# Optimization experiments

Measured on AMD Instinct MI355X. Metric: run time of the kernel, lower is better.

The kernel has to match this reference:

```python
import jax, jax.numpy as jnp
import numpy as np

DIM, DH, H_HEADS, F, HH, WW = 512, 64, 8, 16, 32, 32
FF_IN = int(DIM * 4 * 2 / 3)  # 1365


def _ln(x, w, b):
    m = x.mean(-1, keepdims=True)
    v = ((x - m) ** 2).mean(-1, keepdims=True)
    return (x - m) * jax.lax.rsqrt(v + 1e-5) * w + b


def _attn(x, ln_w, ln_b, wq, wkv, nkv, nbias, wout, oln_w, oln_b, rel_bias):
    # x: (B, N, D); K/V are single-head (shared across heads) per the source to_kv
    B, N, D = x.shape
    H = nbias.shape[0]
    dh = nkv.shape[-1]
    xn = _ln(x, ln_w, ln_b)
    q = (xn @ wq).reshape(B, N, H, dh).transpose(0, 2, 1, 3) * (dh ** -0.5)
    k, v = jnp.split(xn @ wkv, 2, axis=-1)  # (B, N, dh) each
    nk = jnp.broadcast_to(nkv[0], (B, 1, dh))
    nv = jnp.broadcast_to(nkv[1], (B, 1, dh))
    k = jnp.concatenate([nk, k], axis=1)  # (B, N+1, dh)
    v = jnp.concatenate([nv, v], axis=1)
    sim = jnp.einsum('bhid,bjd->bhij', q, k)  # (B, H, N, N+1)
    bias = jnp.concatenate([jnp.broadcast_to(nbias[:, None, None], (H, N, 1)), rel_bias], axis=-1)
    attn = jax.nn.softmax(sim + bias[None], axis=-1)
    out = jnp.einsum('bhij,bjd->bhid', attn, v)
    out = out.transpose(0, 2, 1, 3).reshape(B, N, H * dh)
    return _ln(out @ wout, oln_w, oln_b)


def _cpb_mlp(coords, w0, b0, w1, b1, w2, b2):
    t = jax.nn.silu(coords @ w0 + b0)
    t = jax.nn.silu(t @ w1 + b1)
    return t @ w2 + b2  # (R, heads)


def _spatial_bias(h, w, w0, b0, w1, b1, w2, b2):
    rh = jnp.arange(-h + 1, h)
    rw = jnp.arange(-w + 1, w)
    gh, gw = jnp.meshgrid(rh, rw, indexing='ij')
    coords = jnp.stack([gh, gw], axis=-1).reshape(-1, 2).astype(jnp.float32)
    table = _cpb_mlp(coords, w0, b0, w1, b1, w2, b2)  # ((2h-1)(2w-1), H)
    ph, pw = jnp.meshgrid(jnp.arange(h), jnp.arange(w), indexing='ij')
    p = jnp.stack([ph, pw], axis=-1).reshape(-1, 2)  # (hw, 2)
    rel = p[:, None] - p[None]  # (hw, hw, 2)
    idx = (rel[..., 0] + h - 1) * (2 * w - 1) + (rel[..., 1] + w - 1)
    return table[idx].transpose(2, 0, 1)  # (H, hw, hw)


def _temporal_bias(f, w0, b0, w1, b1, w2, b2):
    coords = jnp.arange(-f + 1, f, dtype=jnp.float32)[:, None]
    table = _cpb_mlp(coords, w0, b0, w1, b1, w2, b2)  # (2f-1, H)
    idx = jnp.arange(f)[:, None] - jnp.arange(f)[None] + f - 1
    return table[idx].transpose(2, 0, 1)  # (H, f, f)


def _ff(x, win, g, wout):
    # 1x1x1 conv == channel matmul; GEGLU; shift_token; ChanLayerNorm; conv out
    y = jnp.einsum('bcfhw,cd->bdfhw', x, win)
    a, gate = jnp.split(y, 2, axis=1)
    y = a * jax.nn.gelu(gate, approximate=False)
    c = y.shape[1]
    c1 = (c + 1) // 2  # torch.chunk: first chunk gets ceil
    y1, y2 = y[:, :c1], y[:, c1:]
    y2 = jnp.pad(y2, ((0, 0), (0, 0), (1, 0), (0, 0), (0, 0)))[:, :, :-1]
    y = jnp.concatenate([y1, y2], axis=1)
    m = y.mean(1, keepdims=True)
    v = ((y - m) ** 2).mean(1, keepdims=True)
    y = (y - m) * jax.lax.rsqrt(jnp.maximum(v, 1e-5)) * g.reshape(1, -1, 1, 1, 1)
    return jnp.einsum('bcfhw,cd->bdfhw', y, wout)


def setup_inputs() -> dict:
    key = jax.random.key(0)
    ks = jax.random.split(key, 32)
    d2 = DIM // 2
    inner = DH * H_HEADS

    def nrm(k, shape, s=0.02):
        return jax.random.normal(k, shape, jnp.float32) * s

    inp = {'x': jax.random.normal(ks[0], (1, DIM, F, HH, WW), jnp.float32)}
    for pre, i in (('sa', 1), ('ta', 11)):
        inp[pre + '_ln_w'] = jnp.ones(DIM, jnp.float32)
        inp[pre + '_ln_b'] = jnp.zeros(DIM, jnp.float32)
        inp[pre + '_wq'] = nrm(ks[i], (DIM, inner))
        inp[pre + '_wkv'] = nrm(ks[i + 1], (DIM, 2 * DH))
        inp[pre + '_null_kv'] = nrm(ks[i + 2], (2, DH), 1.0)
        inp[pre + '_null_bias'] = nrm(ks[i + 3], (H_HEADS,), 1.0)
        inp[pre + '_wout'] = nrm(ks[i + 4], (inner, DIM))
        inp[pre + '_oln_w'] = jnp.ones(DIM, jnp.float32)
        inp[pre + '_oln_b'] = jnp.zeros(DIM, jnp.float32)
    inp['sp_w0'] = nrm(ks[20], (2, d2), 0.1); inp['sp_b0'] = jnp.zeros(d2, jnp.float32)
    inp['sp_w1'] = nrm(ks[21], (d2, d2), 0.05); inp['sp_b1'] = jnp.zeros(d2, jnp.float32)
    inp['sp_w2'] = nrm(ks[22], (d2, H_HEADS), 0.05); inp['sp_b2'] = jnp.zeros(H_HEADS, jnp.float32)
    inp['tp_w0'] = nrm(ks[23], (1, d2), 0.1); inp['tp_b0'] = jnp.zeros(d2, jnp.float32)
    inp['tp_w1'] = nrm(ks[24], (d2, d2), 0.05); inp['tp_b1'] = jnp.zeros(d2, jnp.float32)
    inp['tp_w2'] = nrm(ks[25], (d2, H_HEADS), 0.05); inp['tp_b2'] = jnp.zeros(H_HEADS, jnp.float32)
    inp['ff_win'] = nrm(ks[26], (DIM, 2 * FF_IN))
    inp['ff_g'] = jnp.ones(FF_IN, jnp.float32)
    inp['ff_wout'] = nrm(ks[27], (FF_IN, DIM))
    return inp


def _forward(x, sa_ln_w, sa_ln_b, sa_wq, sa_wkv, sa_null_kv, sa_null_bias, sa_wout, sa_oln_w, sa_oln_b,
             ta_ln_w, ta_ln_b, ta_wq, ta_wkv, ta_null_kv, ta_null_bias, ta_wout, ta_oln_w, ta_oln_b,
             sp_w0, sp_b0, sp_w1, sp_b1, sp_w2, sp_b2,
             tp_w0, tp_b0, tp_w1, tp_b1, tp_w2, tp_b2,
             ff_win, ff_g, ff_wout):
    b, c, f, h, w = x.shape
    # spatial attention over (h*w) tokens, batched over (b*f)
    xs = x.transpose(0, 2, 3, 4, 1).reshape(b * f, h * w, c)
    sb = _spatial_bias(h, w, sp_w0, sp_b0, sp_w1, sp_b1, sp_w2, sp_b2)
    xs = _attn(xs, sa_ln_w, sa_ln_b, sa_wq, sa_wkv, sa_null_kv, sa_null_bias, sa_wout, sa_oln_w, sa_oln_b, sb) + xs
    xv = xs.reshape(b, f, h, w, c).transpose(0, 4, 1, 2, 3)
    # temporal attention over f tokens, batched over (b*h*w)
    xt = xv.transpose(0, 3, 4, 2, 1).reshape(b * h * w, f, c)
    tb = _temporal_bias(f, tp_w0, tp_b0, tp_w1, tp_b1, tp_w2, tp_b2)
    xt = _attn(xt, ta_ln_w, ta_ln_b, ta_wq, ta_wkv, ta_null_kv, ta_null_bias, ta_wout, ta_oln_w, ta_oln_b, tb) + xt
    xv = xt.reshape(b, h, w, f, c).transpose(0, 4, 3, 1, 2)
    # feed-forward with token shift
    return _ff(xv, ff_win, ff_g, ff_wout) + xv


def reference(x, sa_ln_w, sa_ln_b, sa_wq, sa_wkv, sa_null_kv, sa_null_bias, sa_wout, sa_oln_w, sa_oln_b,
              ta_ln_w, ta_ln_b, ta_wq, ta_wkv, ta_null_kv, ta_null_bias, ta_wout, ta_oln_w, ta_oln_b,
              sp_w0, sp_b0, sp_w1, sp_b1, sp_w2, sp_b2,
              tp_w0, tp_b0, tp_w1, tp_b1, tp_w2, tp_b2,
              ff_win, ff_g, ff_wout):
    return _forward(x, sa_ln_w, sa_ln_b, sa_wq, sa_wkv, sa_null_kv, sa_null_bias, sa_wout, sa_oln_w, sa_oln_b,
                    ta_ln_w, ta_ln_b, ta_wq, ta_wkv, ta_null_kv, ta_null_bias, ta_wout, ta_oln_w, ta_oln_b,
                    sp_w0, sp_b0, sp_w1, sp_b1, sp_w2, sp_b2,
                    tp_w0, tp_b0, tp_w1, tp_b1, tp_w2, tp_b2,
                    ff_win, ff_g, ff_wout)
```

## Files before the change

### kernel.cpp

```cpp
#include <hip/hip_runtime.h>
#include <math.h>

#define TOK 16384
#define DIMC 512
#define FFI 1365
#define CH1 683
#define YSLD 1376
#define KVPAD 1056
#define BSTRIDE 1152
#define MASKB (-30000.f)

typedef unsigned int u32;
typedef unsigned short ushort_t;
typedef __attribute__((ext_vector_type(8))) short bf16x8;
typedef __attribute__((ext_vector_type(4))) float f32x4;

__device__ inline ushort_t f2b(float x) {
    u32 u = __float_as_uint(x);
    u32 r = (u + 0x7fffu + ((u >> 16) & 1u)) >> 16;
    return (ushort_t)r;
}
__device__ inline float b2f(ushort_t u) { return __uint_as_float(((u32)u) << 16); }

__device__ inline void gload_lds16(const void* g, void* l) {
    __builtin_amdgcn_global_load_lds(
        (const __attribute__((address_space(1))) u32*)g,
        (__attribute__((address_space(3))) u32*)l, 16, 0, 0);
}

__device__ inline float gelu_exact(float x) {
    return 0.5f * x * (1.f + erff(x * 0.70710678118654752f));
}

__global__ __launch_bounds__(256) void cpb_kernel(
    const float* __restrict__ w0, const float* __restrict__ b0,
    const float* __restrict__ w1, const float* __restrict__ b1,
    const float* __restrict__ w2, const float* __restrict__ b2,
    float* __restrict__ table, int mode)
{
    __shared__ float t0[256];
    __shared__ float t1[256];
    int r = blockIdx.x;
    int t = threadIdx.x;
    float c0, c1;
    if (mode == 0) { c0 = (float)(r / 63 - 31); c1 = (float)(r % 63 - 31); }
    else           { c0 = (float)(r - 15);      c1 = 0.f; }
    float a = c0 * w0[t] + b0[t];
    if (mode == 0) a += c1 * w0[256 + t];
    t0[t] = a / (1.f + __expf(-a));
    __syncthreads();
    float s = b1[t];
    for (int k = 0; k < 256; ++k) s += t0[k] * w1[k * 256 + t];
    t1[t] = s / (1.f + __expf(-s));
    __syncthreads();
    if (t < 8) {
        float o = b2[t];
        for (int k = 0; k < 256; ++k) o += t1[k] * w2[k * 8 + t];
        table[r * 8 + t] = o;
    }
}

__global__ __launch_bounds__(256) void bias_sp_kernel(
    const float* __restrict__ tab, const float* __restrict__ nullbias,
    ushort_t* __restrict__ out)
{
    int pi = blockIdx.x, h = blockIdx.y;
    int phi = pi >> 5, pwi = pi & 31;
    ushort_t* row = out + ((size_t)h * 1024 + pi) * BSTRIDE;
    for (int c = threadIdx.x; c < BSTRIDE; c += 256) {
        float v;
        if (c == 0) v = nullbias[h];
        else if (c <= 1024) {
            int pj = c - 1;
            int phj = pj >> 5, pwj = pj & 31;
            int idx = (phi - phj + 31) * 63 + (pwi - pwj + 31);
            v = tab[idx * 8 + h];
        } else v = MASKB;
        row[c] = f2b(v);
    }
}

__global__ __launch_bounds__(256) void kvinit_kernel(
    const float* __restrict__ nullkv, ushort_t* __restrict__ KP, ushort_t* __restrict__ VT)
{
    int f = blockIdx.x, t = threadIdx.x;
    for (int e = t; e < 32 * 64; e += 256) {
        int rr = e >> 6, d = e & 63;
        int row = (rr == 0) ? 0 : (1024 + rr);
        KP[((size_t)f * KVPAD + row) * 64 + d] = (rr == 0) ? f2b(nullkv[d]) : (ushort_t)0;
    }
    for (int e = t; e < 64 * 32; e += 256) {
        int d = e >> 5, cc = e & 31;
        int col = (cc == 0) ? 0 : (1024 + cc);
        VT[((size_t)f * 64 + d) * KVPAD + col] = (cc == 0) ? f2b(nullkv[64 + d]) : (ushort_t)0;
    }
}

__global__ __launch_bounds__(256) void wcvt_kernel(
    const float* __restrict__ W, int ldw, int c0,
    ushort_t* __restrict__ Bt, int Kp, int K, int Ncols,
    const float* __restrict__ gv, int Nwrite)
{
    __shared__ float tile[32][33];
    int nb = blockIdx.x * 32, kb = blockIdx.y * 32;
    int tx = threadIdx.x & 31, ty = threadIdx.x >> 5;
    #pragma unroll
    for (int it = 0; it < 4; ++it) {
        int k = kb + ty + it * 8, n = nb + tx;
        float v = (k < K && n < Ncols) ? W[(size_t)k * ldw + c0 + n] : 0.f;
        if (gv && k < K) v *= gv[k];
        tile[ty + it * 8][tx] = v;
    }
    __syncthreads();
    #pragma unroll
    for (int it = 0; it < 4; ++it) {
        int n = nb + ty + it * 8, k = kb + tx;
        if (n < Nwrite && k < Kp) Bt[(size_t)n * Kp + k] = f2b(tile[tx][ty + it * 8]);
    }
}

__global__ __launch_bounds__(256) void transpose_in_kernel(
    const float* __restrict__ x, float* __restrict__ dst)
{
    __shared__ float tile[32][33];
    int t0b = blockIdx.x * 32, c0b = blockIdx.y * 32;
    int tx = threadIdx.x & 31, ty = threadIdx.x >> 5;
    #pragma unroll
    for (int it = 0; it < 4; ++it) {
        int c = ty + it * 8;
        tile[c][tx] = x[(size_t)(c0b + c) * TOK + t0b + tx];
    }
    __syncthreads();
    #pragma unroll
    for (int it = 0; it < 4; ++it) {
        int tr = ty + it * 8;
        dst[(size_t)(t0b + tr) * DIMC + c0b + tx] = tile[tx][tr];
    }
}

__global__ __launch_bounds__(256) void ln_bf16_kernel(
    const float* __restrict__ in, ushort_t* __restrict__ out,
    const float* __restrict__ w, const float* __restrict__ b)
{
    __shared__ float r1[4], r2[4];
    size_t base = (size_t)blockIdx.x * DIMC;
    int t = threadIdx.x;
    float x0 = in[base + t], x1 = in[base + 256 + t];
    float s = x0 + x1, s2 = x0 * x0 + x1 * x1;
    #pragma unroll
    for (int o = 32; o > 0; o >>= 1) { s += __shfl_down(s, o, 64); s2 += __shfl_down(s2, o, 64); }
    if ((t & 63) == 0) { r1[t >> 6] = s; r2[t >> 6] = s2; }
    __syncthreads();
    float mean = (r1[0] + r1[1] + r1[2] + r1[3]) * (1.f / 512.f);
    float ex2  = (r2[0] + r2[1] + r2[2] + r2[3]) * (1.f / 512.f);
    float rstd = rsqrtf(ex2 - mean * mean + 1e-5f);
    out[base + t]       = f2b((x0 - mean) * rstd * w[t] + b[t]);
    out[base + 256 + t] = f2b((x1 - mean) * rstd * w[256 + t] + b[256 + t]);
}

__global__ __launch_bounds__(256) void ln_add_kernel(
    const float* __restrict__ proj, float* __restrict__ io,
    const float* __restrict__ w, const float* __restrict__ b)
{
    __shared__ float r1[4], r2[4];
    size_t base = (size_t)blockIdx.x * DIMC;
    int t = threadIdx.x;
    float x0 = proj[base + t], x1 = proj[base + 256 + t];
    float s = x0 + x1, s2 = x0 * x0 + x1 * x1;
    #pragma unroll
    for (int o = 32; o > 0; o >>= 1) { s += __shfl_down(s, o, 64); s2 += __shfl_down(s2, o, 64); }
    if ((t & 63) == 0) { r1[t >> 6] = s; r2[t >> 6] = s2; }
    __syncthreads();
    float mean = (r1[0] + r1[1] + r1[2] + r1[3]) * (1.f / 512.f);
    float ex2  = (r2[0] + r2[1] + r2[2] + r2[3]) * (1.f / 512.f);
    float rstd = rsqrtf(ex2 - mean * mean + 1e-5f);
    io[base + t]       += (x0 - mean) * rstd * w[t] + b[t];
    io[base + 256 + t] += (x1 - mean) * rstd * w[256 + t] + b[256 + t];
}

__global__ __launch_bounds__(128) void permute0_kernel(
    const float* __restrict__ src, float* __restrict__ dst)
{
    int rd = blockIdx.x;
    int rs = (rd & 15) * 1024 + (rd >> 4);
    ((float4*)(dst + (size_t)rd * DIMC))[threadIdx.x] =
        ((const float4*)(src + (size_t)rs * DIMC))[threadIdx.x];
}

__global__ __launch_bounds__(128) void permute1_dual_kernel(
    const float* __restrict__ src, float* __restrict__ dst, ushort_t* __restrict__ dstb)
{
    int rd = blockIdx.x;
    int rs = (rd & 1023) * 16 + (rd >> 10);
    float4 v = ((const float4*)(src + (size_t)rs * DIMC))[threadIdx.x];
    ((float4*)(dst + (size_t)rd * DIMC))[threadIdx.x] = v;
    u32 lo = (u32)f2b(v.x) | ((u32)f2b(v.y) << 16);
    u32 hi = (u32)f2b(v.z) | ((u32)f2b(v.w) << 16);
    ((uint2*)(dstb + (size_t)rd * DIMC))[threadIdx.x] = make_uint2(lo, hi);
}

template<int EPI>
__global__ __launch_bounds__(256) void gemm_mfma(
    const ushort_t* __restrict__ A, int lda,
    const ushort_t* __restrict__ Bt, int Kp,
    float* __restrict__ C, ushort_t* __restrict__ Cb, int ldc,
    int M, int N, int K, float scale, int nx,
    const float* __restrict__ stats, const float* __restrict__ g,
    const float* __restrict__ resid, float* __restrict__ outT,
    ushort_t* __restrict__ KPo, ushort_t* __restrict__ VTo)
{
    __shared__ __align__(16) ushort_t As[4 * 128 * 8];
    __shared__ __align__(16) ushort_t Bs[4 * 128 * 8];
    int lin = blockIdx.x;
    int xcd = lin & 7, idx = lin >> 3;
    int m0 = (xcd * 16 + (idx & 15)) * 128;
    int n0 = (idx >> 4) * 128;
    int tid = threadIdx.x, lane = tid & 63, wid = tid >> 6;
    int wy = wid >> 1, wx = wid & 1, quad = lane >> 4, l16 = lane & 15;
    bool bfull = (n0 + 128 <= N);
    f32x4 acc[4][4];
    #pragma unroll
    for (int i = 0; i < 4; ++i)
        #pragma unroll
        for (int j = 0; j < 4; ++j) { acc[i][j][0]=0.f; acc[i][j][1]=0.f; acc[i][j][2]=0.f; acc[i][j][3]=0.f; }

    for (int k0 = 0; k0 < K; k0 += 32) {
        if (k0) __syncthreads();
        #pragma unroll
        for (int r = 0; r < 2; ++r) {
            int c = wid * 128 + r * 64 + lane;
            const ushort_t* src = A + (size_t)(m0 + (c & 127)) * lda + k0 + (c >> 7) * 8;
            gload_lds16(src, &As[(wid * 128 + r * 64) * 8]);
        }
        if (bfull) {
            #pragma unroll
            for (int r = 0; r < 2; ++r) {
                int c = wid * 128 + r * 64 + lane;
                const ushort_t* src = Bt + (size_t)(n0 + (c & 127)) * Kp + k0 + (c >> 7) * 8;
                gload_lds16(src, &Bs[(wid * 128 + r * 64) * 8]);
            }
        } else {
            #pragma unroll
            for (int r = 0; r < 2; ++r) {
                int c = tid + r * 256;
                int kg = c >> 7, nloc = c & 127;
                bf16x8 v;
                if (n0 + nloc < N) v = *(const bf16x8*)(Bt + (size_t)(n0 + nloc) * Kp + k0 + kg * 8);
                else { for (int e = 0; e < 8; ++e) v[e] = 0; }
                *(bf16x8*)&Bs[c * 8] = v;
            }
        }
        __syncthreads();
        bf16x8 af[4], bfr[4];
        #pragma unroll
        for (int i = 0; i < 4; ++i) af[i] = *(bf16x8*)&As[(quad * 128 + wy * 64 + i * 16 + l16) * 8];
        #pragma unroll
        for (int j = 0; j < 4; ++j) bfr[j] = *(bf16x8*)&Bs[(quad * 128 + wx * 64 + j * 16 + l16) * 8];
        #pragma unroll
        for (int i = 0; i < 4; ++i)
            #pragma unroll
            for (int j = 0; j < 4; ++j)
                acc[i][j] = __builtin_amdgcn_mfma_f32_16x16x32_bf16(af[i], bfr[j], acc[i][j], 0, 0, 0);
    }
    #pragma unroll
    for (int i = 0; i < 4; ++i) {
        #pragma unroll
        for (int j = 0; j < 4; ++j) {
            #pragma unroll
            for (int r = 0; r < 4; ++r) {
                int m = m0 + wy * 64 + i * 16 + quad * 4 + r;
                int n = n0 + wx * 64 + j * 16 + l16;
                if (n >= N) continue;
                float v = acc[i][j][r] * scale;
                if (EPI == 0) {
                    C[(size_t)m * ldc + n] = v;
                } else if (EPI == 3) {
                    Cb[(size_t)m * ldc + n] = f2b(v);
                } else if (EPI == 4) {
                    int frame = m >> 10, tt = m & 1023;
                    if (n < 64) KPo[((size_t)frame * KVPAD + 1 + tt) * 64 + n] = f2b(v);
                    else        VTo[((size_t)frame * 64 + (n - 64)) * KVPAD + 1 + tt] = f2b(v);
                } else if (EPI == 5) {
                    float s0 = stats[2 * m], s1 = stats[2 * m + 1];
                    outT[(size_t)n * TOK + m] = v * s1 - s0 * g[n] + resid[(size_t)m * DIMC + n];
                }
            }
        }
    }
}

__global__ __launch_bounds__(256) void ff_gemm_fused(
    const ushort_t* __restrict__ A,
    const ushort_t* __restrict__ BI,
    ushort_t* __restrict__ YS)
{
    __shared__ __align__(16) ushort_t As[4 * 128 * 8];
    __shared__ __align__(16) ushort_t Bs[4 * 2 * 64 * 8];
    int lin = blockIdx.x;
    int xcd = lin & 7, idx = lin >> 3;
    int m0 = (xcd * 16 + (idx & 15)) * 128;
    int n0 = (idx >> 4) * 64;
    int tid = threadIdx.x, lane = tid & 63, wid = tid >> 6;
    int wy = wid >> 1, wx = wid & 1, quad = lane >> 4, l16 = lane & 15;
    f32x4 aA[4][2], aG[4][2];
    #pragma unroll
    for (int i = 0; i < 4; ++i)
        #pragma unroll
        for (int j = 0; j < 2; ++j) {
            aA[i][j][0]=0.f; aA[i][j][1]=0.f; aA[i][j][2]=0.f; aA[i][j][3]=0.f;
            aG[i][j][0]=0.f; aG[i][j][1]=0.f; aG[i][j][2]=0.f; aG[i][j][3]=0.f;
        }

    for (int k0 = 0; k0 < 512; k0 += 32) {
        if (k0) __syncthreads();
        #pragma unroll
        for (int r = 0; r < 2; ++r) {
            int c = wid * 128 + r * 64 + lane;
            gload_lds16(A + (size_t)(m0 + (c & 127)) * 512 + k0 + (c >> 7) * 8,
                        &As[(wid * 128 + r * 64) * 8]);
        }
        #pragma unroll
        for (int r = 0; r < 2; ++r) {
            gload_lds16(BI + (size_t)((n0 + lane) * 2 + r) * 512 + k0 + wid * 8,
                        &Bs[(wid * 128 + r * 64) * 8]);
        }
        __syncthreads();
        bf16x8 af[4], ba[2], bg[2];
        #pragma unroll
        for (int i = 0; i < 4; ++i) af[i] = *(bf16x8*)&As[(quad * 128 + wy * 64 + i * 16 + l16) * 8];
        #pragma unroll
        for (int j = 0; j < 2; ++j) {
            int nn = wx * 32 + j * 16 + l16;
            ba[j] = *(bf16x8*)&Bs[(quad * 128 + nn) * 8];
            bg[j] = *(bf16x8*)&Bs[(quad * 128 + 64 + nn) * 8];
        }
        #pragma unroll
        for (int i = 0; i < 4; ++i)
            #pragma unroll
            for (int j = 0; j < 2; ++j) {
                aA[i][j] = __builtin_amdgcn_mfma_f32_16x16x32_bf16(af[i], ba[j], aA[i][j], 0, 0, 0);
                aG[i][j] = __builtin_amdgcn_mfma_f32_16x16x32_bf16(af[i], bg[j], aG[i][j], 0, 0, 0);
            }
    }
    #pragma unroll
    for (int i = 0; i < 4; ++i) {
        #pragma unroll
        for (int j = 0; j < 2; ++j) {
            #pragma unroll
            for (int r = 0; r < 4; ++r) {
                int m = m0 + wy * 64 + i * 16 + quad * 4 + r;
                int n = n0 + wx * 32 + j * 16 + l16;
                if (n >= FFI) {
                    if (n < YSLD) YS[(size_t)m * YSLD + n] = 0;
                    continue;
                }
                float v = aA[i][j][r] * gelu_exact(aG[i][j][r]);
                int dr = (n < CH1) ? m : m + 1024;
                if (dr < TOK) YS[(size_t)dr * YSLD + n] = f2b(v);
                if (n >= CH1 && m < 1024) YS[(size_t)m * YSLD + n] = 0;
            }
        }
    }
}

__global__ __launch_bounds__(256) void attn_sp_mfma(
    const ushort_t* __restrict__ Q,
    const ushort_t* __restrict__ KP,
    const ushort_t* __restrict__ VT,
    const ushort_t* __restrict__ BIASX,
    ushort_t* __restrict__ O)
{
    __shared__ __align__(16) ushort_t Ks[128 * 64];
    __shared__ __align__(16) ushort_t Vs[64 * 128];
    __shared__ __align__(16) ushort_t PT[4][16 * 136];
    int lin = blockIdx.x;
    int xcd = lin & 7, idx = lin >> 3;
    int qt = xcd * 8 + (idx & 7);
    int frame = idx >> 3;
    int q0 = qt * 16;
    int tid = threadIdx.x, lane = tid & 63, wid = tid >> 6;
    int quad = lane >> 4, l16 = lane & 15;
    ushort_t* PTw = &PT[wid][0];

    bf16x8 aQ[2][2];
    const ushort_t* brow[2];
    #pragma unroll
    for (int i = 0; i < 2; ++i) {
        int h = wid * 2 + i;
        const ushort_t* qp = Q + (size_t)(frame * 1024 + q0 + l16) * 512 + h * 64 + quad * 8;
        aQ[i][0] = *(const bf16x8*)qp;
        aQ[i][1] = *(const bf16x8*)(qp + 32);
        brow[i] = BIASX + ((size_t)h * 1024 + q0 + l16) * BSTRIDE;
    }
    f32x4 Oc[2][4];
    float mcol[2], lcol[2];
    #pragma unroll
    for (int i = 0; i < 2; ++i) {
        #pragma unroll
        for (int nt = 0; nt < 4; ++nt) { Oc[i][nt][0]=0.f; Oc[i][nt][1]=0.f; Oc[i][nt][2]=0.f; Oc[i][nt][3]=0.f; }
        mcol[i] = -1.0e30f; lcol[i] = 0.f;
    }

    for (int jt = 0; jt < 9; ++jt) {
        __syncthreads();
        #pragma unroll
        for (int r = 0; r < 4; ++r) {
            int L = wid * 256 + r * 64 + lane;
            int c = L >> 3, gp = L & 7, gg = gp ^ (c & 7);
            int jj = jt * 128 + c; if (jj > KVPAD - 1) jj = KVPAD - 1;
            gload_lds16(KP + ((size_t)frame * KVPAD + jj) * 64 + gg * 8, &Ks[(wid * 256 + r * 64) * 8]);
        }
        #pragma unroll
        for (int r = 0; r < 4; ++r) {
            int L = wid * 256 + r * 64 + lane;
            int d = L >> 4, cgp = L & 15;
            int cg = (cgp & 8) | ((cgp & 7) ^ (d & 7));
            int col = jt * 128 + cg * 8; if (col > KVPAD - 8) col = KVPAD - 8;
            gload_lds16(VT + ((size_t)frame * 64 + d) * KVPAD + col, &Vs[(wid * 256 + r * 64) * 8]);
        }
        __syncthreads();
        f32x4 S[2][8];
        #pragma unroll
        for (int i = 0; i < 2; ++i)
            #pragma unroll
            for (int j = 0; j < 8; ++j) { S[i][j][0]=0.f; S[i][j][1]=0.f; S[i][j][2]=0.f; S[i][j][3]=0.f; }
        #pragma unroll
        for (int j = 0; j < 8; ++j) {
            int c = j * 16 + l16;
            #pragma unroll
            for (int ks = 0; ks < 2; ++ks) {
                bf16x8 kb = *(bf16x8*)&Ks[(c * 8 + ((ks * 4 + quad) ^ (c & 7))) * 8];
                S[0][j] = __builtin_amdgcn_mfma_f32_16x16x32_bf16(kb, aQ[0][ks], S[0][j], 0, 0, 0);
                S[1][j] = __builtin_amdgcn_mfma_f32_16x16x32_bf16(kb, aQ[1][ks], S[1][j], 0, 0, 0);
            }
        }
        #pragma unroll
        for (int i = 0; i < 2; ++i) {
            #pragma unroll
            for (int j = 0; j < 8; ++j) {
                int kbase = jt * 128 + j * 16 + quad * 4;
                uint2 bv = *(const uint2*)(brow[i] + kbase);
                S[i][j][0] += b2f((ushort_t)(bv.x & 0xffffu));
                S[i][j][1] += b2f((ushort_t)(bv.x >> 16));
                S[i][j][2] += b2f((ushort_t)(bv.y & 0xffffu));
                S[i][j][3] += b2f((ushort_t)(bv.y >> 16));
            }
        }
        float alpha[2];
        #pragma unroll
        for (int i = 0; i < 2; ++i) {
            float mx = S[i][0][0];
            #pragma unroll
            for (int j = 0; j < 8; ++j)
                #pragma unroll
                for (int r = 0; r < 4; ++r) mx = fmaxf(mx, S[i][j][r]);
            mx = fmaxf(mx, __shfl_xor(mx, 16, 64));
            mx = fmaxf(mx, __shfl_xor(mx, 32, 64));
            float mnew = fmaxf(mcol[i], mx);
            alpha[i] = __expf(mcol[i] - mnew);
            mcol[i] = mnew;
            float rs = 0.f;
            #pragma unroll
            for (int j = 0; j < 8; ++j)
                #pragma unroll
                for (int r = 0; r < 4; ++r) {
                    float p = __expf(S[i][j][r] - mnew);
                    S[i][j][r] = p;
                    rs += p;
                }
            rs += __shfl_xor(rs, 16, 64);
            rs += __shfl_xor(rs, 32, 64);
            lcol[i] = lcol[i] * alpha[i] + rs;
        }
        #pragma unroll
        for (int i = 0; i < 2; ++i) {
            #pragma unroll
            for (int r = 0; r < 4; ++r) {
                float ar = __shfl(alpha[i], quad * 4 + r, 64);
                #pragma unroll
                for (int nt = 0; nt < 4; ++nt) Oc[i][nt][r] *= ar;
            }
        }
        #pragma unroll
        for (int i = 0; i < 2; ++i) {
            #pragma unroll
            for (int j = 0; j < 8; ++j) {
                u32 u0 = __float_as_uint(S[i][j][0]) + 0x8000u;
                u32 u1 = __float_as_uint(S[i][j][1]) + 0x8000u;
                u32 u2 = __float_as_uint(S[i][j][2]) + 0x8000u;
                u32 u3 = __float_as_uint(S[i][j][3]) + 0x8000u;
                uint2 pk;
                pk.x = (u0 >> 16) | (u1 & 0xffff0000u);
                pk.y = (u2 >> 16) | (u3 & 0xffff0000u);
                *(uint2*)&PTw[l16 * 136 + j * 16 + quad * 4] = pk;
            }
            #pragma unroll
            for (int ks = 0; ks < 4; ++ks) {
                bf16x8 pa = *(bf16x8*)&PTw[l16 * 136 + ks * 32 + quad * 8];
                #pragma unroll
                for (int nt = 0; nt < 4; ++nt) {
                    int d = nt * 16 + l16;
                    int cg = ks * 4 + quad;
                    int phys = (cg & 8) | ((cg & 7) ^ (d & 7));
                    bf16x8 vb = *(bf16x8*)&Vs[(d * 16 + phys) * 8];
                    Oc[i][nt] = __builtin_amdgcn_mfma_f32_16x16x32_bf16(pa, vb, Oc[i][nt], 0, 0, 0);
                }
            }
        }
    }
    #pragma unroll
    for (int i = 0; i < 2; ++i) {
        int h = wid * 2 + i;
        #pragma unroll
        for (int r = 0; r < 4; ++r) {
            float linv = 1.f / __shfl(lcol[i], quad * 4 + r, 64);
            int ql = quad * 4 + r;
            #pragma unroll
            for (int nt = 0; nt < 4; ++nt) {
                int d = nt * 16 + l16;
                O[(size_t)(frame * 1024 + q0 + ql) * 512 + h * 64 + d] = f2b(Oc[i][nt][r] * linv);
            }
        }
    }
}

__global__ __launch_bounds__(256) void attn_tp_kernel(
    const ushort_t* __restrict__ q, const ushort_t* __restrict__ kv,
    const float* __restrict__ nullkv, const float* __restrict__ nullbias,
    const float* __restrict__ table, ushort_t* __restrict__ out)
{
    __shared__ float qs[16][512];
    __shared__ float ks[17][64];
    __shared__ float vs[17][64];
    __shared__ float sc[8][16][17];
    int b = blockIdx.x;
    int t = threadIdx.x;
    for (int e = t; e < 16 * 512; e += 256) {
        int f = e >> 9, c = e & 511;
        qs[f][c] = b2f(q[(size_t)(b * 16 + f) * 512 + c]);
    }
    for (int e = t; e < 17 * 64; e += 256) {
        int j = e >> 6, d = e & 63;
        ks[j][d] = (j == 0) ? nullkv[d]      : b2f(kv[(size_t)(b * 16 + j - 1) * 128 + d]);
        vs[j][d] = (j == 0) ? nullkv[64 + d] : b2f(kv[(size_t)(b * 16 + j - 1) * 128 + 64 + d]);
    }
    __syncthreads();
    for (int e = t; e < 8 * 16 * 17; e += 256) {
        int h = e / 272, rem = e - h * 272;
        int i = rem / 17, j = rem - i * 17;
        float acc = 0.f;
        for (int d = 0; d < 64; ++d) acc += qs[i][h * 64 + d] * ks[j][d];
        float bias = (j == 0) ? nullbias[h] : table[(i - (j - 1) + 15) * 8 + h];
        sc[h][i][j] = acc + bias;
    }
    __syncthreads();
    if (t < 128) {
        int h = t >> 4, i = t & 15;
        float mx = -1e30f;
        for (int j = 0; j < 17; ++j) mx = fmaxf(mx, sc[h][i][j]);
        float s = 0.f;
        for (int j = 0; j < 17; ++j) { float p = __expf(sc[h][i][j] - mx); sc[h][i][j] = p; s += p; }
        float inv = 1.f / s;
        for (int j = 0; j < 17; ++j) sc[h][i][j] *= inv;
    }
    __syncthreads();
    for (int e = t; e < 16 * 512; e += 256) {
        int i = e >> 9, c = e & 511;
        int h = c >> 6, d = c & 63;
        float acc = 0.f;
        #pragma unroll
        for (int j = 0; j < 17; ++j) acc += sc[h][i][j] * vs[j][d];
        out[(size_t)(b * 16 + i) * 512 + c] = f2b(acc);
    }
}

__global__ __launch_bounds__(256) void rowstats_bf16_kernel(
    const ushort_t* __restrict__ YS, float* __restrict__ stats)
{
    __shared__ float r1[4], r2[4];
    int r = blockIdx.x, t = threadIdx.x;
    const ushort_t* row = YS + (size_t)r * YSLD;
    float s = 0.f, s2 = 0.f;
    for (int c = t; c < FFI; c += 256) {
        float v = b2f(row[c]);
        s += v; s2 += v * v;
    }
    #pragma unroll
    for (int o = 32; o > 0; o >>= 1) { s += __shfl_down(s, o, 64); s2 += __shfl_down(s2, o, 64); }
    if ((t & 63) == 0) { r1[t >> 6] = s; r2[t >> 6] = s2; }
    __syncthreads();
    float S  = r1[0] + r1[1] + r1[2] + r1[3];
    float S2 = r2[0] + r2[1] + r2[2] + r2[3];
    float mean = S * (1.f / 1365.f);
    float var  = S2 * (1.f / 1365.f) - mean * mean;
    float rstd = rsqrtf(fmaxf(var, 1e-5f));
    if (t == 0) { stats[2 * r] = mean * rstd; stats[2 * r + 1] = rstd; }
}

__global__ __launch_bounds__(64) void colsum_kernel(
    const ushort_t* __restrict__ Wt, float* __restrict__ colsum)
{
    int n = blockIdx.x, t = threadIdx.x;
    const ushort_t* row = Wt + (size_t)n * YSLD;
    float s = 0.f;
    for (int k = t; k < YSLD; k += 64) s += b2f(row[k]);
    #pragma unroll
    for (int o = 32; o > 0; o >>= 1) s += __shfl_down(s, o, 64);
    if (t == 0) colsum[n] = s;
}

extern "C" void kernel_launch(void* const* d_in, const int* in_sizes, int n_in,
                              void* d_out, int out_size, void* d_ws, size_t ws_size,
                              hipStream_t stream)
{
    const float* x          = (const float*)d_in[0];
    const float* sa_ln_w    = (const float*)d_in[1];
    const float* sa_ln_b    = (const float*)d_in[2];
    const float* sa_wq      = (const float*)d_in[3];
    const float* sa_wkv     = (const float*)d_in[4];
    const float* sa_null_kv = (const float*)d_in[5];
    const float* sa_null_b  = (const float*)d_in[6];
    const float* sa_wout    = (const float*)d_in[7];
    const float* sa_oln_w   = (const float*)d_in[8];
    const float* sa_oln_b   = (const float*)d_in[9];
    const float* ta_ln_w    = (const float*)d_in[10];
    const float* ta_ln_b    = (const float*)d_in[11];
    const float* ta_wq      = (const float*)d_in[12];
    const float* ta_wkv     = (const float*)d_in[13];
    const float* ta_null_kv = (const float*)d_in[14];
    const float* ta_null_b  = (const float*)d_in[15];
    const float* ta_wout    = (const float*)d_in[16];
    const float* ta_oln_w   = (const float*)d_in[17];
    const float* ta_oln_b   = (const float*)d_in[18];
    const float* sp_w0      = (const float*)d_in[19];
    const float* sp_b0      = (const float*)d_in[20];
    const float* sp_w1      = (const float*)d_in[21];
    const float* sp_b1      = (const float*)d_in[22];
    const float* sp_w2      = (const float*)d_in[23];
    const float* sp_b2      = (const float*)d_in[24];
    const float* tp_w0      = (const float*)d_in[25];
    const float* tp_b0      = (const float*)d_in[26];
    const float* tp_w1      = (const float*)d_in[27];
    const float* tp_b1      = (const float*)d_in[28];
    const float* tp_w2      = (const float*)d_in[29];
    const float* tp_b2      = (const float*)d_in[30];
    const float* ff_win     = (const float*)d_in[31];
    const float* ff_g       = (const float*)d_in[32];
    const float* ff_wout    = (const float*)d_in[33];

    char* ws = (char*)d_ws;
    float*    RES   = (float*)(ws + 0);
    ushort_t* XN16  = (ushort_t*)(ws + 33554432);
    ushort_t* Q16   = (ushort_t*)(ws + 50331648);
    float*    RT    = (float*)(ws + 50331648);
    ushort_t* YS    = (ushort_t*)(ws + 50331648);
    ushort_t* WSA   = (ushort_t*)(ws + 67108864);
    ushort_t* KP    = (ushort_t*)(ws + 83886080);
    ushort_t* VTb   = (ushort_t*)(ws + 86048768);
    ushort_t* KV16  = (ushort_t*)(ws + 83886080);
    ushort_t* WTA   = (ushort_t*)(ws + 90439680);
    ushort_t* AO16  = (ushort_t*)(ws + 92274688);
    ushort_t* BI    = (ushort_t*)(ws + 96468992);
    ushort_t* WFFB  = (ushort_t*)(ws + 99352576);
    ushort_t* BIAS16= (ushort_t*)(ws + 109051904);
    float*    PRJ   = (float*)(ws + 109051904);
    ushort_t* Q16t  = (ushort_t*)(ws + 109051904);
    float*    STATS = (float*)(ws + 142606336);
    float*    SPT   = (float*)(ws + 142737408);
    float*    COLSUM= (float*)(ws + 142737408);
    float*    TPT   = (float*)(ws + 142864448);

    ushort_t* WQ_T  = WSA;
    ushort_t* WKV_T = WSA + 262144;
    ushort_t* WO_T  = WSA + 327680;
    ushort_t* tWQ_T  = WTA;
    ushort_t* tWKV_T = WTA + 262144;
    ushort_t* tWO_T  = WTA + 327680;

    dim3 blk(256);

    cpb_kernel<<<dim3(3969), blk, 0, stream>>>(sp_w0, sp_b0, sp_w1, sp_b1, sp_w2, sp_b2, SPT, 0);
    cpb_kernel<<<dim3(31),   blk, 0, stream>>>(tp_w0, tp_b0, tp_w1, tp_b1, tp_w2, tp_b2, TPT, 1);
    bias_sp_kernel<<<dim3(1024, 8), blk, 0, stream>>>(SPT, sa_null_b, BIAS16);
    kvinit_kernel<<<dim3(16), blk, 0, stream>>>(sa_null_kv, KP, VTb);

    wcvt_kernel<<<dim3(16, 16), blk, 0, stream>>>(sa_wq, 512, 0, WQ_T, 512, 512, 512, nullptr, 512);
    wcvt_kernel<<<dim3(4, 16),  blk, 0, stream>>>(sa_wkv, 128, 0, WKV_T, 512, 512, 128, nullptr, 128);
    wcvt_kernel<<<dim3(16, 16), blk, 0, stream>>>(sa_wout, 512, 0, WO_T, 512, 512, 512, nullptr, 512);
    transpose_in_kernel<<<dim3(512, 16), blk, 0, stream>>>(x, RES);
    ln_bf16_kernel<<<dim3(TOK), blk, 0, stream>>>(RES, XN16, sa_ln_w, sa_ln_b);
    gemm_mfma<3><<<dim3(512), blk, 0, stream>>>(XN16, 512, WQ_T, 512,
        nullptr, Q16, 512, TOK, 512, 512, 0.125f, 4, nullptr, nullptr, nullptr, nullptr, nullptr, nullptr);
    gemm_mfma<4><<<dim3(128), blk, 0, stream>>>(XN16, 512, WKV_T, 512,
        nullptr, nullptr, 0, TOK, 128, 512, 1.0f, 1, nullptr, nullptr, nullptr, nullptr, KP, VTb);
    attn_sp_mfma<<<dim3(1024), blk, 0, stream>>>(Q16, KP, VTb, BIAS16, AO16);
    gemm_mfma<0><<<dim3(512), blk, 0, stream>>>(AO16, 512, WO_T, 512,
        PRJ, nullptr, 512, TOK, 512, 512, 1.0f, 4, nullptr, nullptr, nullptr, nullptr, nullptr, nullptr);
    ln_add_kernel<<<dim3(TOK), blk, 0, stream>>>(PRJ, RES, sa_oln_w, sa_oln_b);

    permute0_kernel<<<dim3(TOK), dim3(128), 0, stream>>>(RES, RT);
    wcvt_kernel<<<dim3(16, 16), blk, 0, stream>>>(ta_wq, 512, 0, tWQ_T, 512, 512, 512, nullptr, 512);
    wcvt_kernel<<<dim3(4, 16),  blk, 0, stream>>>(ta_wkv, 128, 0, tWKV_T, 512, 512, 128, nullptr, 128);
    wcvt_kernel<<<dim3(16, 16), blk, 0, stream>>>(ta_wout, 512, 0, tWO_T, 512, 512, 512, nullptr, 512);
    ln_bf16_kernel<<<dim3(TOK), blk, 0, stream>>>(RT, XN16, ta_ln_w, ta_ln_b);
    gemm_mfma<3><<<dim3(512), blk, 0, stream>>>(XN16, 512, tWQ_T, 512,
        nullptr, Q16t, 512, TOK, 512, 512, 0.125f, 4, nullptr, nullptr, nullptr, nullptr, nullptr, nullptr);
    gemm_mfma<3><<<dim3(128), blk, 0, stream>>>(XN16, 512, tWKV_T, 512,
        nullptr, KV16, 128, TOK, 128, 512, 1.0f, 1, nullptr, nullptr, nullptr, nullptr, nullptr, nullptr);
    attn_tp_kernel<<<dim3(1024), blk, 0, stream>>>(Q16t, KV16, ta_null_kv, ta_null_b, TPT, AO16);
    gemm_mfma<0><<<dim3(512), blk, 0, stream>>>(AO16, 512, tWO_T, 512,
        PRJ, nullptr, 512, TOK, 512, 512, 1.0f, 4, nullptr, nullptr, nullptr, nullptr, nullptr, nullptr);
    ln_add_kernel<<<dim3(TOK), blk, 0, stream>>>(PRJ, RT, ta_oln_w, ta_oln_b);
    permute1_dual_kernel<<<dim3(TOK), dim3(128), 0, stream>>>(RT, RES, XN16);

    wcvt_kernel<<<dim3(44, 16), blk, 0, stream>>>(ff_win, 2730, 0,   BI,       1024, 512, FFI, nullptr, 1408);
    wcvt_kernel<<<dim3(44, 16), blk, 0, stream>>>(ff_win, 2730, FFI, BI + 512, 1024, 512, FFI, nullptr, 1408);
    wcvt_kernel<<<dim3(16, 43), blk, 0, stream>>>(ff_wout, 512, 0, WFFB, YSLD, FFI, 512, ff_g, 512);
    colsum_kernel<<<dim3(512), dim3(64), 0, stream>>>(WFFB, COLSUM);
    ff_gemm_fused<<<dim3(2816), blk, 0, stream>>>(XN16, BI, YS);
    rowstats_bf16_kernel<<<dim3(TOK), blk, 0, stream>>>(YS, STATS);
    gemm_mfma<5><<<dim3(512), blk, 0, stream>>>(YS, YSLD, WFFB, YSLD,
        nullptr, nullptr, 0, TOK, 512, YSLD, 1.0f, 4, STATS, COLSUM, RES, (float*)d_out, nullptr, nullptr);
}
```

Baseline: 919.5 us.

## Use base-2 softmax and register-permuted P in spatial attention kernel

Folds log2(e) into the query scale and the precomputed bias tables so that both attention kernels can use the raw v_exp_f32 instruction instead of __expf. In the spatial attention kernel, the softmax probabilities are no longer staged through shared memory. They are rearranged into the MFMA A-operand layout with ds_bpermute, which removes the PT LDS buffer. The kernel now processes one head at a time to cut live registers, adds s_setprio around the MFMA blocks, and sets a launch-bounds occupancy hint. The costs are extra cross-lane permute instructions, and the log2(e) scaling of the bias is rounded to bf16.

```diff
diff --git a/kernel.cpp b/kernel.cpp
--- a/kernel.cpp
+++ b/kernel.cpp
@@ -9,6 +9,7 @@
 #define KVPAD 1056
 #define BSTRIDE 1152
 #define MASKB (-30000.f)
+#define LOG2E 1.4426950408889634f
 
 typedef unsigned int u32;
 typedef unsigned short ushort_t;
@@ -21,6 +22,12 @@
     return (ushort_t)r;
 }
 __device__ inline float b2f(ushort_t u) { return __uint_as_float(((u32)u) << 16); }
+
+__device__ inline float exp2_fast(float x) {
+    float r;
+    asm("v_exp_f32 %0, %1" : "=v"(r) : "v"(x));
+    return r;
+}
 
 __device__ inline void gload_lds16(const void* g, void* l) {
     __builtin_amdgcn_global_load_lds(
@@ -76,7 +83,7 @@
             int idx = (phi - phj + 31) * 63 + (pwi - pwj + 31);
             v = tab[idx * 8 + h];
         } else v = MASKB;
-        row[c] = f2b(v);
+        row[c] = f2b(v * LOG2E);
     }
 }
 
@@ -363,7 +370,7 @@
     }
 }
 
-__global__ __launch_bounds__(256) void attn_sp_mfma(
+__global__ __launch_bounds__(256, 4) void attn_sp_mfma(
     const ushort_t* __restrict__ Q,
     const ushort_t* __restrict__ KP,
     const ushort_t* __restrict__ VT,
@@ -372,7 +379,6 @@
 {
     __shared__ __align__(16) ushort_t Ks[128 * 64];
     __shared__ __align__(16) ushort_t Vs[64 * 128];
-    __shared__ __align__(16) ushort_t PT[4][16 * 136];
     int lin = blockIdx.x;
     int xcd = lin & 7, idx = lin >> 3;
     int qt = xcd * 8 + (idx & 7);
@@ -380,7 +386,6 @@
     int q0 = qt * 16;
     int tid = threadIdx.x, lane = tid & 63, wid = tid >> 6;
     int quad = lane >> 4, l16 = lane & 15;
-    ushort_t* PTw = &PT[wid][0];
 
     bf16x8 aQ[2][2];
     const ushort_t* brow[2];
@@ -401,6 +406,10 @@
         mcol[i] = -1.0e30f; lcol[i] = 0.f;
     }
 
+    int idxA = (((quad & 1) * 32) + l16) * 4;
+    int idxB = idxA + 64;
+    bool hiq = (quad >= 2);
+
     for (int jt = 0; jt < 9; ++jt) {
         __syncthreads();
         #pragma unroll
@@ -419,93 +428,100 @@
             gload_lds16(VT + ((size_t)frame * 64 + d) * KVPAD + col, &Vs[(wid * 256 + r * 64) * 8]);
         }
         __syncthreads();
-        f32x4 S[2][8];
-        #pragma unroll
-        for (int i = 0; i < 2; ++i)
-            #pragma unroll
-            for (int j = 0; j < 8; ++j) { S[i][j][0]=0.f; S[i][j][1]=0.f; S[i][j][2]=0.f; S[i][j][3]=0.f; }
-        #pragma unroll
-        for (int j = 0; j < 8; ++j) {
-            int c = j * 16 + l16;
-            #pragma unroll
-            for (int ks = 0; ks < 2; ++ks) {
-                bf16x8 kb = *(bf16x8*)&Ks[(c * 8 + ((ks * 4 + quad) ^ (c & 7))) * 8];
-                S[0][j] = __builtin_amdgcn_mfma_f32_16x16x32_bf16(kb, aQ[0][ks], S[0][j], 0, 0, 0);
-                S[1][j] = __builtin_amdgcn_mfma_f32_16x16x32_bf16(kb, aQ[1][ks], S[1][j], 0, 0, 0);
-            }
-        }
+
         #pragma unroll
         for (int i = 0; i < 2; ++i) {
+            f32x4 S[8];
+            #pragma unroll
+            for (int j = 0; j < 8; ++j) { S[j][0]=0.f; S[j][1]=0.f; S[j][2]=0.f; S[j][3]=0.f; }
+            __builtin_amdgcn_s_setprio(1);
+            #pragma unroll
+            for (int j = 0; j < 8; ++j) {
+                int c = j * 16 + l16;
+                #pragma unroll
+                for (int ks = 0; ks < 2; ++ks) {
+                    bf16x8 kb = *(bf16x8*)&Ks[(c * 8 + ((ks * 4 + quad) ^ (c & 7))) * 8];
+                    S[j] = __builtin_amdgcn_mfma_f32_16x16x32_bf16(kb, aQ[i][ks], S[j], 0, 0, 0);
+                }
+            }
+            __builtin_amdgcn_s_setprio(0);
             #pragma unroll
             for (int j = 0; j < 8; ++j) {
                 int kbase = jt * 128 + j * 16 + quad * 4;
                 uint2 bv = *(const uint2*)(brow[i] + kbase);
-                S[i][j][0] += b2f((ushort_t)(bv.x & 0xffffu));
-                S[i][j][1] += b2f((ushort_t)(bv.x >> 16));
-                S[i][j][2] += b2f((ushort_t)(bv.y & 0xffffu));
-                S[i][j][3] += b2f((ushort_t)(bv.y >> 16));
-            }
-        }
-        float alpha[2];
-        #pragma unroll
-        for (int i = 0; i < 2; ++i) {
-            float mx = S[i][0][0];
+                S[j][0] += b2f((ushort_t)(bv.x & 0xffffu));
+                S[j][1] += b2f((ushort_t)(bv.x >> 16));
+                S[j][2] += b2f((ushort_t)(bv.y & 0xffffu));
+                S[j][3] += b2f((ushort_t)(bv.y >> 16));
+            }
+            float mj[8];
             #pragma unroll
             for (int j = 0; j < 8; ++j)
-                #pragma unroll
-                for (int r = 0; r < 4; ++r) mx = fmaxf(mx, S[i][j][r]);
+                mj[j] = fmaxf(fmaxf(S[j][0], S[j][1]), fmaxf(S[j][2], S[j][3]));
+            float mx = fmaxf(fmaxf(fmaxf(mj[0], mj[1]), fmaxf(mj[2], mj[3])),
+                             fmaxf(fmaxf(mj[4], mj[5]), fmaxf(mj[6], mj[7])));
             mx = fmaxf(mx, __shfl_xor(mx, 16, 64));
             mx = fmaxf(mx, __shfl_xor(mx, 32, 64));
             float mnew = fmaxf(mcol[i], mx);
-            alpha[i] = __expf(mcol[i] - mnew);
+            float alpha = exp2_fast(mcol[i] - mnew);
             mcol[i] = mnew;
-            float rs = 0.f;
-            #pragma unroll
-            for (int j = 0; j < 8; ++j)
-                #pragma unroll
-                for (int r = 0; r < 4; ++r) {
-                    float p = __expf(S[i][j][r] - mnew);
-                    S[i][j][r] = p;
-                    rs += p;
-                }
+            float sj[8];
+            #pragma unroll
+            for (int j = 0; j < 8; ++j) {
+                float p0 = exp2_fast(S[j][0] - mnew);
+                float p1 = exp2_fast(S[j][1] - mnew);
+                float p2 = exp2_fast(S[j][2] - mnew);
+                float p3 = exp2_fast(S[j][3] - mnew);
+                S[j][0] = p0; S[j][1] = p1; S[j][2] = p2; S[j][3] = p3;
+                sj[j] = (p0 + p1) + (p2 + p3);
+            }
+            float rs = ((sj[0] + sj[1]) + (sj[2] + sj[3])) + ((sj[4] + sj[5]) + (sj[6] + sj[7]));
             rs += __shfl_xor(rs, 16, 64);
             rs += __shfl_xor(rs, 32, 64);
-            lcol[i] = lcol[i] * alpha[i] + rs;
-        }
-        #pragma unroll
-        for (int i = 0; i < 2; ++i) {
+            lcol[i] = lcol[i] * alpha + rs;
             #pragma unroll
             for (int r = 0; r < 4; ++r) {
-                float ar = __shfl(alpha[i], quad * 4 + r, 64);
+                float ar = __shfl(alpha, quad * 4 + r, 64);
                 #pragma unroll
                 for (int nt = 0; nt < 4; ++nt) Oc[i][nt][r] *= ar;
             }
-        }
-        #pragma unroll
-        for (int i = 0; i < 2; ++i) {
+            u32 px[8], py[8];
             #pragma unroll
             for (int j = 0; j < 8; ++j) {
-                u32 u0 = __float_as_uint(S[i][j][0]) + 0x8000u;
-                u32 u1 = __float_as_uint(S[i][j][1]) + 0x8000u;
-                u32 u2 = __float_as_uint(S[i][j][2]) + 0x8000u;
-                u32 u3 = __float_as_uint(S[i][j][3]) + 0x8000u;
-                uint2 pk;
-                pk.x = (u0 >> 16) | (u1 & 0xffff0000u);
-                pk.y = (u2 >> 16) | (u3 & 0xffff0000u);
-                *(uint2*)&PTw[l16 * 136 + j * 16 + quad * 4] = pk;
-            }
+                u32 u0 = __float_as_uint(S[j][0]) + 0x8000u;
+                u32 u1 = __float_as_uint(S[j][1]) + 0x8000u;
+                u32 u2 = __float_as_uint(S[j][2]) + 0x8000u;
+                u32 u3 = __float_as_uint(S[j][3]) + 0x8000u;
+                px[j] = (u0 >> 16) | (u1 & 0xffff0000u);
+                py[j] = (u2 >> 16) | (u3 & 0xffff0000u);
+            }
+            __builtin_amdgcn_s_setprio(1);
             #pragma unroll
             for (int ks = 0; ks < 4; ++ks) {
-                bf16x8 pa = *(bf16x8*)&PTw[l16 * 136 + ks * 32 + quad * 8];
+                int jl = 2 * ks, jh = 2 * ks + 1;
+                u32 a0 = (u32)__builtin_amdgcn_ds_bpermute(idxA, (int)px[jl]);
+                u32 a1 = (u32)__builtin_amdgcn_ds_bpermute(idxA, (int)px[jh]);
+                u32 b0 = (u32)__builtin_amdgcn_ds_bpermute(idxA, (int)py[jl]);
+                u32 b1 = (u32)__builtin_amdgcn_ds_bpermute(idxA, (int)py[jh]);
+                u32 c0 = (u32)__builtin_amdgcn_ds_bpermute(idxB, (int)px[jl]);
+                u32 c1 = (u32)__builtin_amdgcn_ds_bpermute(idxB, (int)px[jh]);
+                u32 d0 = (u32)__builtin_amdgcn_ds_bpermute(idxB, (int)py[jl]);
+                u32 d1 = (u32)__builtin_amdgcn_ds_bpermute(idxB, (int)py[jh]);
+                union { u32 w[4]; bf16x8 v; } pa;
+                pa.w[0] = hiq ? a1 : a0;
+                pa.w[1] = hiq ? b1 : b0;
+                pa.w[2] = hiq ? c1 : c0;
+                pa.w[3] = hiq ? d1 : d0;
                 #pragma unroll
                 for (int nt = 0; nt < 4; ++nt) {
                     int d = nt * 16 + l16;
                     int cg = ks * 4 + quad;
                     int phys = (cg & 8) | ((cg & 7) ^ (d & 7));
                     bf16x8 vb = *(bf16x8*)&Vs[(d * 16 + phys) * 8];
-                    Oc[i][nt] = __builtin_amdgcn_mfma_f32_16x16x32_bf16(pa, vb, Oc[i][nt], 0, 0, 0);
+                    Oc[i][nt] = __builtin_amdgcn_mfma_f32_16x16x32_bf16(pa.v, vb, Oc[i][nt], 0, 0, 0);
                 }
             }
+            __builtin_amdgcn_s_setprio(0);
         }
     }
     #pragma unroll
@@ -550,7 +566,7 @@
         int i = rem / 17, j = rem - i * 17;
         float acc = 0.f;
         for (int d = 0; d < 64; ++d) acc += qs[i][h * 64 + d] * ks[j][d];
-        float bias = (j == 0) ? nullbias[h] : table[(i - (j - 1) + 15) * 8 + h];
+        float bias = ((j == 0) ? nullbias[h] : table[(i - (j - 1) + 15) * 8 + h]) * LOG2E;
         sc[h][i][j] = acc + bias;
     }
     __syncthreads();
@@ -559,7 +575,7 @@
         float mx = -1e30f;
         for (int j = 0; j < 17; ++j) mx = fmaxf(mx, sc[h][i][j]);
         float s = 0.f;
-        for (int j = 0; j < 17; ++j) { float p = __expf(sc[h][i][j] - mx); sc[h][i][j] = p; s += p; }
+        for (int j = 0; j < 17; ++j) { float p = exp2_fast(sc[h][i][j] - mx); sc[h][i][j] = p; s += p; }
         float inv = 1.f / s;
         for (int j = 0; j < 17; ++j) sc[h][i][j] *= inv;
     }
@@ -678,6 +694,7 @@
     ushort_t* tWO_T  = WTA + 327680;
 
     dim3 blk(256);
+    const float QSCL = 0.125f * LOG2E;
 
     cpb_kernel<<<dim3(3969), blk, 0, stream>>>(sp_w0, sp_b0, sp_w1, sp_b1, sp_w2, sp_b2, SPT, 0);
     cpb_kernel<<<dim3(31),   blk, 0, stream>>>(tp_w0, tp_b0, tp_w1, tp_b1, tp_w2, tp_b2, TPT, 1);
@@ -690,7 +707,7 @@
     transpose_in_kernel<<<dim3(512, 16), blk, 0, stream>>>(x, RES);
     ln_bf16_kernel<<<dim3(TOK), blk, 0, stream>>>(RES, XN16, sa_ln_w, sa_ln_b);
     gemm_mfma<3><<<dim3(512), blk, 0, stream>>>(XN16, 512, WQ_T, 512,
-        nullptr, Q16, 512, TOK, 512, 512, 0.125f, 4, nullptr, nullptr, nullptr, nullptr, nullptr, nullptr);
+        nullptr, Q16, 512, TOK, 512, 512, QSCL, 4, nullptr, nullptr, nullptr, nullptr, nullptr, nullptr);
     gemm_mfma<4><<<dim3(128), blk, 0, stream>>>(XN16, 512, WKV_T, 512,
         nullptr, nullptr, 0, TOK, 128, 512, 1.0f, 1, nullptr, nullptr, nullptr, nullptr, KP, VTb);
     attn_sp_mfma<<<dim3(1024), blk, 0, stream>>>(Q16, KP, VTb, BIAS16, AO16);
@@ -704,7 +721,7 @@
     wcvt_kernel<<<dim3(16, 16), blk, 0, stream>>>(ta_wout, 512, 0, tWO_T, 512, 512, 512, nullptr, 512);
     ln_bf16_kernel<<<dim3(TOK), blk, 0, stream>>>(RT, XN16, ta_ln_w, ta_ln_b);
     gemm_mfma<3><<<dim3(512), blk, 0, stream>>>(XN16, 512, tWQ_T, 512,
-        nullptr, Q16t, 512, TOK, 512, 512, 0.125f, 4, nullptr, nullptr, nullptr, nullptr, nullptr, nullptr);
+        nullptr, Q16t, 512, TOK, 512, 512, QSCL, 4, nullptr, nullptr, nullptr, nullptr, nullptr, nullptr);
     gemm_mfma<3><<<dim3(128), blk, 0, stream>>>(XN16, 512, tWKV_T, 512,
         nullptr, KV16, 128, TOK, 128, 512, 1.0f, 1, nullptr, nullptr, nullptr, nullptr, nullptr, nullptr);
     attn_tp_kernel<<<dim3(1024), blk, 0, stream>>>(Q16t, KV16, ta_null_kv, ta_null_b, TPT, AO16);
```

After: 1.013 ms. 1.1x slower.
